# Optimization experiments

Hardware: AMD Instinct MI355X
Metric: run time of the kernel (lower is better)

Reference implementation:

```python
import jax, jax.numpy as jnp
import numpy as np

B, D, S = 16, 64, 2048


def setup_inputs() -> dict:
    key = jax.random.key(0)
    kq, kk, kv, km = jax.random.split(key, 4)
    q = jax.random.normal(kq, (B, D, S), dtype=jnp.float32)
    k = jax.random.normal(kk, (B, D, S), dtype=jnp.float32)
    v = jax.random.normal(kv, (B, D, S), dtype=jnp.float32)
    # boolean mask over the [B, Sq, Sk] score matrix (True -> filled with -1000)
    mask = jax.random.bernoulli(km, 0.1, (B, S, S))
    return {"q": q, "k": k, "v": v, "mask": mask}


def reference(q, k, v, mask):
    dim = jnp.asarray(D, dtype=q.dtype)
    # scores[b, s, t] = sum_d q[b, d, s] * k[b, d, t] / sqrt(D)
    scores = jnp.einsum("bds,bdt->bst", q, k) / jnp.sqrt(dim)
    scores = jnp.where(mask, jnp.asarray(-1000.0, dtype=scores.dtype), scores)
    # NOTE: softmax over dim=1 (the QUERY axis), faithful to nn.Softmax(dim=1)
    attn = jax.nn.softmax(scores, axis=1)
    # out[b, s, d] = sum_t attn[b, s, t] * v[b, d, t]
    out = jnp.einsum("bst,bdt->bsd", attn, v)
    return out
```

## Files before the change

### kernel.cpp

```cpp
#include <hip/hip_runtime.h>
#include <hip/hip_bf16.h>
#include <stdint.h>


namespace {
constexpr int B = 16;
constexpr int D = 64;
constexpr int S = 2048;
constexpr float SCALE = 0.125f;

typedef __attribute__((ext_vector_type(8))) short short8;
typedef __attribute__((ext_vector_type(4))) float f32x4;

constexpr size_t WS_FLAG  = 0;
constexpr size_t WS_LINV  = 256;
constexpr size_t WS_LPART = 256 + 131072;
constexpr size_t WS_QT    = 655616;
constexpr size_t WS_KT    = 4849920;
constexpr size_t WS_VB    = 9044224;
constexpr size_t WS_MPACK = 13238528;
constexpr size_t WS_OPART = 21627136;
constexpr size_t NEED_OLD = 13238528;
constexpr size_t NEED_T1  = 21627136;
constexpr size_t NEED_T2  = 38404352;
}

__device__ __forceinline__ bool mask_at(const void* mask, int mode, size_t idx) {
    if (mode == 1) return ((const int*)mask)[idx] != 0;
    if (mode == 2) return ((const float*)mask)[idx] != 0.0f;
    return ((const unsigned char*)mask)[idx] != 0;
}

__device__ __forceinline__ uint16_t f2bf(float f) {
    unsigned int u = __float_as_uint(f);
    unsigned int r = (u + 0x7fffu + ((u >> 16) & 1u)) >> 16;
    return (uint16_t)r;
}
__device__ __forceinline__ unsigned int pack2(float a, float b) {
    return (unsigned int)f2bf(a) | ((unsigned int)f2bf(b) << 16);
}

__device__ __forceinline__ int swz(int row, int colByte) {
    return row * 128 + (colByte ^ ((row & 7) << 4));
}

__device__ __forceinline__ void gll16(const void* g, void* l) {
    __builtin_amdgcn_global_load_lds(
        (const __attribute__((address_space(1))) void*)g,
        (__attribute__((address_space(3))) void*)l, 16, 0, 0);
}

__device__ __forceinline__ void stage_tile(const char* srcRows, size_t rowStrideB,
                                           unsigned char* dst, int tid) {
    const int lane = tid & 63, w = tid >> 6;
    const int lrow = lane >> 3;
    const int slot = (lane & 7) ^ lrow;
    #pragma unroll
    for (int c = 0; c < 2; ++c) {
        const int row = 16 * w + 8 * c + lrow;
        gll16(srcRows + (size_t)row * rowStrideB + slot * 16,
              dst + (16 * w + 8 * c) * 128);
    }
}

__device__ __forceinline__ f32x4 mfma16(short8 a, short8 b, f32x4 c) {
    return __builtin_amdgcn_mfma_f32_16x16x32_bf16(a, b, c, 0, 0, 0);
}

__global__ void probe_mask_kernel(const unsigned char* __restrict__ mask,
                                  int* __restrict__ flag)
{
    __shared__ int c0s, c123s;
    if (threadIdx.x == 0) { c0s = 0; c123s = 0; }
    __syncthreads();
    int c0 = 0, c123 = 0;
    for (int f = threadIdx.x; f < 65536; f += 256) {
        const int nz = (mask[f] != 0) ? 1 : 0;
        if ((f & 3) == 0) c0 += nz; else c123 += nz;
    }
    atomicAdd(&c0s, c0);
    atomicAdd(&c123s, c123);
    __syncthreads();
    if (threadIdx.x == 0) {
        int mode = 0;
        if (c123s == 0) mode = 1;
        else if (c0s == 0) mode = 2;
        *flag = mode;
    }
}

__global__ __launch_bounds__(256, 2)
void prep_kernel(const float* __restrict__ q, const float* __restrict__ k,
                 const float* __restrict__ v,
                 uint16_t* __restrict__ qT, uint16_t* __restrict__ kT,
                 uint16_t* __restrict__ vb)
{
    __shared__ float ts[64][65];
    const int tid = threadIdx.x;
    const int s0 = blockIdx.x * 64;
    const int b  = blockIdx.y;

    if (blockIdx.z == 2) {
        const int d = tid >> 2, c = tid & 3;
        const float* row = v + ((size_t)b * D + d) * S + s0 + c * 16;
        uint16_t*   orow = vb + ((size_t)b * D + d) * S + s0 + c * 16;
        #pragma unroll
        for (int i = 0; i < 4; ++i) {
            float4 v4 = *(const float4*)(row + 4 * i);
            uint16_t t4[4] = {f2bf(v4.x), f2bf(v4.y), f2bf(v4.z), f2bf(v4.w)};
            *(uint2*)(orow + 4 * i) = *(const uint2*)t4;
        }
        return;
    }

    const float* src = blockIdx.z ? k : q;
    uint16_t*    dst = blockIdx.z ? kT : qT;
    {
        const int d = tid >> 2, c = tid & 3;
        const float* row = src + ((size_t)b * D + d) * S + s0 + c * 16;
        #pragma unroll
        for (int i = 0; i < 4; ++i) {
            float4 v4 = *(const float4*)(row + 4 * i);
            ts[c * 16 + 4 * i + 0][d] = v4.x;
            ts[c * 16 + 4 * i + 1][d] = v4.y;
            ts[c * 16 + 4 * i + 2][d] = v4.z;
            ts[c * 16 + 4 * i + 3][d] = v4.w;
        }
    }
    __syncthreads();
    {
        const int srow = tid >> 2, p = tid & 3;
        uint16_t tmp[16];
        #pragma unroll
        for (int j = 0; j < 16; ++j) tmp[j] = f2bf(ts[srow][p * 16 + j]);
        uint16_t* drow = dst + ((size_t)b * S + s0 + srow) * 64 + p * 16;
        *(uint4*)drow       = ((const uint4*)tmp)[0];
        *((uint4*)drow + 1) = ((const uint4*)tmp)[1];
    }
}

__global__ __launch_bounds__(256, 4)
void pass1_kernel(const uint16_t* __restrict__ qT, const uint16_t* __restrict__ kT,
                  const void* __restrict__ mask, const int* __restrict__ flagp,
                  float* __restrict__ lpart, unsigned long long* __restrict__ mpackT)
{
    __shared__ __align__(16) unsigned char ksb[64 * 128];
    __shared__ __align__(16) unsigned char qsb[2][64 * 128];
    __shared__ unsigned short mbits[64][4];
    __shared__ float red[4][64];

    const int tid = threadIdx.x;
    const int lane = tid & 63, w = tid >> 6;
    const int l = lane & 15, hh = lane >> 4;
    const int t0 = blockIdx.x * 64;
    const int chunk = blockIdx.y;
    const int b = blockIdx.z;
    const int mode = *flagp;

    const int row_m = tid >> 2, cq = tid & 3;
    const size_t mrow_base = ((size_t)b * S + row_m) * S + t0 + cq * 16;

    int4  mr4[4];
    uint4 mr1;
    auto load_mtile = [&](int sbase) {
        if (mode != 0) {
            const int4* p = (const int4*)((const int*)mask + mrow_base + (size_t)sbase * S);
            mr4[0] = p[0]; mr4[1] = p[1]; mr4[2] = p[2]; mr4[3] = p[3];
        } else {
            mr1 = *(const uint4*)((const unsigned char*)mask + mrow_base + (size_t)sbase * S);
        }
    };
    auto pack_mtile = [&]() -> unsigned int {
        unsigned int bits = 0;
        if (mode != 0) {
            #pragma unroll
            for (int i = 0; i < 4; ++i) {
                bits |= (mr4[i].x ? 1u : 0u) << (4 * i + 0);
                bits |= (mr4[i].y ? 1u : 0u) << (4 * i + 1);
                bits |= (mr4[i].z ? 1u : 0u) << (4 * i + 2);
                bits |= (mr4[i].w ? 1u : 0u) << (4 * i + 3);
            }
        } else {
            const unsigned int u[4] = {mr1.x, mr1.y, mr1.z, mr1.w};
            #pragma unroll
            for (int c = 0; c < 4; ++c) {
                bits |= ((u[c] & 0x000000FFu) ? 1u : 0u) << (4 * c + 0);
                bits |= ((u[c] & 0x0000FF00u) ? 1u : 0u) << (4 * c + 1);
                bits |= ((u[c] & 0x00FF0000u) ? 1u : 0u) << (4 * c + 2);
                bits |= ((u[c] & 0xFF000000u) ? 1u : 0u) << (4 * c + 3);
            }
        }
        return bits;
    };

    stage_tile((const char*)(kT + ((size_t)b * S + t0) * 64), 128, ksb, tid);
    stage_tile((const char*)(qT + ((size_t)b * S + chunk * 512) * 64), 128, qsb[0], tid);
    load_mtile(chunk * 512);

    float colacc[4] = {0.f, 0.f, 0.f, 0.f};

    for (int it = 0; it < 8; ++it) {
        const int cur = it & 1;
        const int sbase = chunk * 512 + it * 64;

        __syncthreads();

        const unsigned int bits = pack_mtile();
        mbits[row_m][cq] = (unsigned short)bits;

        __syncthreads();

        if (tid < 64) {
            const unsigned long long word =
                (unsigned long long)mbits[tid][0]
                | ((unsigned long long)mbits[tid][1] << 16)
                | ((unsigned long long)mbits[tid][2] << 32)
                | ((unsigned long long)mbits[tid][3] << 48);
            mpackT[((size_t)b * 32 + (t0 >> 6)) * S + sbase + tid] = word;
        }

        if (it < 7) {
            stage_tile((const char*)(qT + ((size_t)b * S + sbase + 64) * 64), 128,
                       qsb[cur ^ 1], tid);
            load_mtile(sbase + 64);
        }

        short8 A0 = *(const short8*)&qsb[cur][swz(16 * w + l, 0  + hh * 16)];
        short8 A1 = *(const short8*)&qsb[cur][swz(16 * w + l, 64 + hh * 16)];
        const int srow_l = 16 * w + 4 * hh;

        #pragma unroll
        for (int tf = 0; tf < 4; ++tf) {
            const short8 B0 = *(const short8*)&ksb[swz(tf * 16 + l, 0  + hh * 16)];
            const short8 B1 = *(const short8*)&ksb[swz(tf * 16 + l, 64 + hh * 16)];
            f32x4 c4 = {0.f, 0.f, 0.f, 0.f};
            c4 = mfma16(A0, B0, c4);
            c4 = mfma16(A1, B1, c4);
            #pragma unroll
            for (int r = 0; r < 4; ++r) {
                if (!((mbits[srow_l + r][tf] >> l) & 1))
                    colacc[tf] += __expf(c4[r] * SCALE);
            }
        }
    }

    #pragma unroll
    for (int tf = 0; tf < 4; ++tf) {
        colacc[tf] += __shfl_xor(colacc[tf], 16);
        colacc[tf] += __shfl_xor(colacc[tf], 32);
    }
    __syncthreads();
    if (lane < 16) {
        #pragma unroll
        for (int tf = 0; tf < 4; ++tf) red[w][tf * 16 + lane] = colacc[tf];
    }
    __syncthreads();
    if (tid < 64) {
        const float s = red[0][tid] + red[1][tid] + red[2][tid] + red[3][tid];
        lpart[(size_t)chunk * (B * S) + (size_t)b * S + t0 + tid] = s;
    }
}

__global__ void linv_kernel(const float* __restrict__ lpart, float* __restrict__ linv)
{
    const int i = blockIdx.x * 256 + threadIdx.x;
    const float s = lpart[i] + lpart[B * S + i] + lpart[2 * B * S + i] + lpart[3 * B * S + i];
    linv[i] = 1.0f / s;
}

__global__ __launch_bounds__(256, 2)
void pass2_kernel(const uint16_t* __restrict__ qT, const uint16_t* __restrict__ kT,
                  const uint16_t* __restrict__ vb,
                  const unsigned long long* __restrict__ mpackT,
                  const float* __restrict__ linv, float* __restrict__ dst, int tspan)
{
    __shared__ __align__(16) unsigned char qsb[64 * 128];
    __shared__ __align__(16) unsigned char ksb[2][64 * 128];
    __shared__ __align__(16) unsigned char vsb[2][64 * 128];
    __shared__ __align__(16) unsigned char ptb[64 * 128];
    __shared__ unsigned long long mrow2[2][64];
    __shared__ float linv_s[2][64];

    const int tid = threadIdx.x;
    const int lane = tid & 63, w = tid >> 6;
    const int l = lane & 15, hh = lane >> 4;
    const int s0 = blockIdx.x * 64;
    const int tc = blockIdx.y;
    const int b = blockIdx.z;
    const int t_begin = tc * tspan;
    const int niter = tspan / 64;
    float* outp = dst + (size_t)tc * (B * S * D);

    stage_tile((const char*)(qT + ((size_t)b * S + s0) * 64), 128, qsb, tid);
    stage_tile((const char*)(kT + ((size_t)b * S + t_begin) * 64), 128, ksb[0], tid);
    stage_tile((const char*)(vb + (size_t)b * D * S + t_begin), (size_t)S * 2, vsb[0], tid);
    if (tid < 64) {
        mrow2[0][tid]  = mpackT[((size_t)b * 32 + (t_begin >> 6)) * S + s0 + tid];
        linv_s[0][tid] = linv[(size_t)b * S + t_begin + tid];
    }
    __syncthreads();

    short8 QB[4][2];
    #pragma unroll
    for (int sf = 0; sf < 4; ++sf)
        #pragma unroll
        for (int kh = 0; kh < 2; ++kh)
            QB[sf][kh] = *(const short8*)&qsb[swz(sf * 16 + l, kh * 64 + hh * 16)];

    f32x4 oacc[4];
    #pragma unroll
    for (int df = 0; df < 4; ++df) oacc[df] = (f32x4){0.f, 0.f, 0.f, 0.f};

    for (int i = 0; i < niter; ++i) {
        const int cur = i & 1, nxt = cur ^ 1;
        const int t0 = t_begin + i * 64;

        short8 KA0 = *(const short8*)&ksb[cur][swz(16 * w + l, 0  + hh * 16)];
        short8 KA1 = *(const short8*)&ksb[cur][swz(16 * w + l, 64 + hh * 16)];
        float lv[4];
        #pragma unroll
        for (int r = 0; r < 4; ++r) lv[r] = linv_s[cur][16 * w + 4 * hh + r];

        #pragma unroll
        for (int sf = 0; sf < 4; ++sf) {
            f32x4 c4 = {0.f, 0.f, 0.f, 0.f};
            c4 = mfma16(KA0, QB[sf][0], c4);
            c4 = mfma16(KA1, QB[sf][1], c4);
            const unsigned long long bits = mrow2[cur][sf * 16 + l];
            float pv[4];
            #pragma unroll
            for (int r = 0; r < 4; ++r) {
                const int tloc = 16 * w + 4 * hh + r;
                pv[r] = ((bits >> tloc) & 1ull) ? 0.f : __expf(c4[r] * SCALE) * lv[r];
            }
            const int row = sf * 16 + l;
            const int cb = (32 * w + 8 * hh);
            *(uint2*)&ptb[row * 128 + (cb ^ ((row & 7) << 4))] =
                make_uint2(pack2(pv[0], pv[1]), pack2(pv[2], pv[3]));
        }
        __syncthreads();

        if (i + 1 < niter) {
            const int tn = t0 + 64;
            stage_tile((const char*)(kT + ((size_t)b * S + tn) * 64), 128, ksb[nxt], tid);
            stage_tile((const char*)(vb + (size_t)b * D * S + tn), (size_t)S * 2, vsb[nxt], tid);
            if (tid < 64) {
                const unsigned long long mw =
                    mpackT[((size_t)b * 32 + (tn >> 6)) * S + s0 + tid];
                const float lw = linv[(size_t)b * S + tn + tid];
                mrow2[nxt][tid]  = mw;
                linv_s[nxt][tid] = lw;
            }
        }

        short8 PA0 = *(const short8*)&ptb[swz(16 * w + l, 0  + hh * 16)];
        short8 PA1 = *(const short8*)&ptb[swz(16 * w + l, 64 + hh * 16)];
        #pragma unroll
        for (int df = 0; df < 4; ++df) {
            short8 VB0 = *(const short8*)&vsb[cur][swz(df * 16 + l, 0  + hh * 16)];
            short8 VB1 = *(const short8*)&vsb[cur][swz(df * 16 + l, 64 + hh * 16)];
            oacc[df] = mfma16(PA0, VB0, oacc[df]);
            oacc[df] = mfma16(PA1, VB1, oacc[df]);
        }
        __syncthreads();
    }

    #pragma unroll
    for (int df = 0; df < 4; ++df)
        #pragma unroll
        for (int r = 0; r < 4; ++r)
            outp[((size_t)b * S + s0 + 16 * w + 4 * hh + r) * D + df * 16 + l] = oacc[df][r];
}

__global__ void opart_reduce_kernel(const float* __restrict__ p, float* __restrict__ out)
{
    const size_t i = ((size_t)blockIdx.x * 256 + threadIdx.x) * 4;
    float4 a = *(const float4*)(p + i);
    float4 b = *(const float4*)(p + (size_t)B * S * D + i);
    *(float4*)(out + i) = make_float4(a.x + b.x, a.y + b.y, a.z + b.z, a.w + b.w);
}

__global__ __launch_bounds__(256, 2)
void transpose_cvt_kernel(const float* __restrict__ q, const float* __restrict__ k,
                          uint16_t* __restrict__ qT, uint16_t* __restrict__ kT)
{
    __shared__ float ts[64][65];
    const int tid = threadIdx.x;
    const int s0 = blockIdx.x * 64;
    const int b  = blockIdx.y;
    const float* src = blockIdx.z ? k : q;
    uint16_t*    dst = blockIdx.z ? kT : qT;
    {
        const int d = tid >> 2, c = tid & 3;
        const float* row = src + ((size_t)b * D + d) * S + s0 + c * 16;
        #pragma unroll
        for (int i = 0; i < 4; ++i) {
            float4 v4 = *(const float4*)(row + 4 * i);
            ts[c * 16 + 4 * i + 0][d] = v4.x;
            ts[c * 16 + 4 * i + 1][d] = v4.y;
            ts[c * 16 + 4 * i + 2][d] = v4.z;
            ts[c * 16 + 4 * i + 3][d] = v4.w;
        }
    }
    __syncthreads();
    {
        const int srow = tid >> 2, p = tid & 3;
        uint16_t tmp[16];
        #pragma unroll
        for (int j = 0; j < 16; ++j) tmp[j] = f2bf(ts[srow][p * 16 + j]);
        uint16_t* drow = dst + ((size_t)b * S + s0 + srow) * 64 + p * 16;
        *(uint4*)drow       = ((const uint4*)tmp)[0];
        *((uint4*)drow + 1) = ((const uint4*)tmp)[1];
    }
}

__global__ void cvt_v_kernel(const float* __restrict__ v, uint16_t* __restrict__ vb)
{
    const size_t i = ((size_t)blockIdx.x * 256 + threadIdx.x) * 4;
    float4 v4 = *(const float4*)(v + i);
    uint16_t t4[4] = {f2bf(v4.x), f2bf(v4.y), f2bf(v4.z), f2bf(v4.w)};
    *(uint2*)(vb + i) = *(const uint2*)t4;
}

__global__ __launch_bounds__(256, 2)
void pass1_old_kernel(const uint16_t* __restrict__ qT, const uint16_t* __restrict__ kT,
                      const void* __restrict__ mask, const int* __restrict__ flagp,
                      float* __restrict__ lpart)
{
    __shared__ __align__(16) unsigned char ksb[64 * 128];
    __shared__ __align__(16) unsigned char qsb[64 * 128];
    __shared__ float red[4][64];
    const int tid = threadIdx.x;
    const int lane = tid & 63, w = tid >> 6;
    const int l = lane & 15, hh = lane >> 4;
    const int t0 = blockIdx.x * 64;
    const int chunk = blockIdx.y;
    const int b = blockIdx.z;
    const int mode = *flagp;
    const size_t mbase = (size_t)b * S * S;

    stage_tile((const char*)(kT + ((size_t)b * S + t0) * 64), 128, ksb, tid);
    __syncthreads();
    short8 BF[4][2];
    #pragma unroll
    for (int tf = 0; tf < 4; ++tf)
        #pragma unroll
        for (int kh = 0; kh < 2; ++kh)
            BF[tf][kh] = *(const short8*)&ksb[swz(tf * 16 + l, kh * 64 + hh * 16)];
    float colacc[4] = {0.f, 0.f, 0.f, 0.f};
    for (int it = 0; it < 8; ++it) {
        const int sbase = chunk * 512 + it * 64;
        __syncthreads();
        stage_tile((const char*)(qT + ((size_t)b * S + sbase) * 64), 128, qsb, tid);
        __syncthreads();
        short8 A0 = *(const short8*)&qsb[swz(16 * w + l, 0  + hh * 16)];
        short8 A1 = *(const short8*)&qsb[swz(16 * w + l, 64 + hh * 16)];
        #pragma unroll
        for (int tf = 0; tf < 4; ++tf) {
            f32x4 c4 = {0.f, 0.f, 0.f, 0.f};
            c4 = mfma16(A0, BF[tf][0], c4);
            c4 = mfma16(A1, BF[tf][1], c4);
            const int t = t0 + tf * 16 + l;
            const int srow = sbase + 16 * w + 4 * hh;
            #pragma unroll
            for (int r = 0; r < 4; ++r)
                if (!mask_at(mask, mode, mbase + (size_t)(srow + r) * S + t))
                    colacc[tf] += __expf(c4[r] * SCALE);
        }
    }
    #pragma unroll
    for (int tf = 0; tf < 4; ++tf) {
        colacc[tf] += __shfl_xor(colacc[tf], 16);
        colacc[tf] += __shfl_xor(colacc[tf], 32);
    }
    if (lane < 16) {
        #pragma unroll
        for (int tf = 0; tf < 4; ++tf) red[w][tf * 16 + lane] = colacc[tf];
    }
    __syncthreads();
    if (tid < 64) {
        const float s = red[0][tid] + red[1][tid] + red[2][tid] + red[3][tid];
        lpart[(size_t)chunk * (B * S) + (size_t)b * S + t0 + tid] = s;
    }
}

__global__ __launch_bounds__(256, 2)
void pass2_old_kernel(const uint16_t* __restrict__ qT, const uint16_t* __restrict__ kT,
                      const uint16_t* __restrict__ vb, const void* __restrict__ mask,
                      const int* __restrict__ flagp, const float* __restrict__ linv,
                      float* __restrict__ out)
{
    __shared__ __align__(16) unsigned char qsb[64 * 128];
    __shared__ __align__(16) unsigned char ksb[64 * 128];
    __shared__ __align__(16) unsigned char vsb[64 * 128];
    __shared__ __align__(16) unsigned char ptb[64 * 128];
    __shared__ unsigned short mbits[64][4];
    __shared__ float linv_s[64];
    const int tid = threadIdx.x;
    const int lane = tid & 63, w = tid >> 6;
    const int l = lane & 15, hh = lane >> 4;
    const int s0 = blockIdx.x * 64;
    const int b = blockIdx.y;
    const int mode = *flagp;
    const size_t mbase = (size_t)b * S * S;

    stage_tile((const char*)(qT + ((size_t)b * S + s0) * 64), 128, qsb, tid);
    __syncthreads();
    short8 QB[4][2];
    #pragma unroll
    for (int sf = 0; sf < 4; ++sf)
        #pragma unroll
        for (int kh = 0; kh < 2; ++kh)
            QB[sf][kh] = *(const short8*)&qsb[swz(sf * 16 + l, kh * 64 + hh * 16)];
    f32x4 oacc[4];
    #pragma unroll
    for (int df = 0; df < 4; ++df) oacc[df] = (f32x4){0.f, 0.f, 0.f, 0.f};

    for (int t0 = 0; t0 < S; t0 += 64) {
        stage_tile((const char*)(kT + ((size_t)b * S + t0) * 64), 128, ksb, tid);
        stage_tile((const char*)(vb + (size_t)b * D * S + t0), (size_t)S * 2, vsb, tid);
        {
            const int srow = tid >> 2, c = tid & 3;
            const size_t base = mbase + (size_t)(s0 + srow) * S + t0 + c * 16;
            unsigned int bits = 0;
            #pragma unroll
            for (int j = 0; j < 16; ++j)
                bits |= (mask_at(mask, mode, base + j) ? 1u : 0u) << j;
            mbits[srow][c] = (unsigned short)bits;
        }
        if (tid < 64) linv_s[tid] = linv[(size_t)b * S + t0 + tid];
        __syncthreads();

        short8 KA0 = *(const short8*)&ksb[swz(16 * w + l, 0  + hh * 16)];
        short8 KA1 = *(const short8*)&ksb[swz(16 * w + l, 64 + hh * 16)];
        float lv[4];
        #pragma unroll
        for (int r = 0; r < 4; ++r) lv[r] = linv_s[16 * w + 4 * hh + r];
        #pragma unroll
        for (int sf = 0; sf < 4; ++sf) {
            f32x4 c4 = {0.f, 0.f, 0.f, 0.f};
            c4 = mfma16(KA0, QB[sf][0], c4);
            c4 = mfma16(KA1, QB[sf][1], c4);
            const unsigned int mb = (unsigned int)mbits[sf * 16 + l][w] >> (4 * hh);
            float pv[4];
            #pragma unroll
            for (int r = 0; r < 4; ++r)
                pv[r] = ((mb >> r) & 1u) ? 0.f : __expf(c4[r] * SCALE) * lv[r];
            const int row = sf * 16 + l;
            const int cb = (32 * w + 8 * hh);
            *(uint2*)&ptb[row * 128 + (cb ^ ((row & 7) << 4))] =
                make_uint2(pack2(pv[0], pv[1]), pack2(pv[2], pv[3]));
        }
        __syncthreads();
        short8 PA0 = *(const short8*)&ptb[swz(16 * w + l, 0  + hh * 16)];
        short8 PA1 = *(const short8*)&ptb[swz(16 * w + l, 64 + hh * 16)];
        #pragma unroll
        for (int df = 0; df < 4; ++df) {
            short8 VB0 = *(const short8*)&vsb[swz(df * 16 + l, 0  + hh * 16)];
            short8 VB1 = *(const short8*)&vsb[swz(df * 16 + l, 64 + hh * 16)];
            oacc[df] = mfma16(PA0, VB0, oacc[df]);
            oacc[df] = mfma16(PA1, VB1, oacc[df]);
        }
        __syncthreads();
    }
    #pragma unroll
    for (int df = 0; df < 4; ++df)
        #pragma unroll
        for (int r = 0; r < 4; ++r)
            out[((size_t)b * S + s0 + 16 * w + 4 * hh + r) * D + df * 16 + l] = oacc[df][r];
}

__global__ __launch_bounds__(256, 2)
void colsum_fb(const float* __restrict__ q, const float* __restrict__ k,
               const void* __restrict__ mask, const int* __restrict__ flagp,
               float* __restrict__ lsums)
{
    __shared__ __align__(16) float qs[128][68];
    __shared__ __align__(16) float ks[64][68];
    __shared__ float lred[32][66];
    const int tid = threadIdx.x;
    const int b = blockIdx.y;
    const int t0 = blockIdx.x * 64;
    const int mode = *flagp;
    {
        const int tl = tid & 63, d0 = tid >> 6;
        #pragma unroll
        for (int i = 0; i < 16; ++i) { const int d = d0 + i * 4; ks[tl][d] = k[(b * D + d) * S + t0 + tl]; }
    }
    const int tq = tid & 7, sq = tid >> 3;
    float lacc[8];
    #pragma unroll
    for (int j = 0; j < 8; ++j) lacc[j] = 0.f;
    const size_t mbase = (size_t)b * S * S;
    for (int s0 = 0; s0 < S; s0 += 128) {
        __syncthreads();
        {
            const int sl = tid & 127, d0 = tid >> 7;
            #pragma unroll
            for (int i = 0; i < 32; ++i) { const int d = d0 + i * 2; qs[sl][d] = q[(b * D + d) * S + s0 + sl]; }
        }
        __syncthreads();
        float acc[4][8];
        #pragma unroll
        for (int jj = 0; jj < 4; ++jj)
            #pragma unroll
            for (int j = 0; j < 8; ++j) acc[jj][j] = 0.f;
        #pragma unroll
        for (int dblk = 0; dblk < 16; ++dblk) {
            float4 q4[4];
            #pragma unroll
            for (int jj = 0; jj < 4; ++jj) q4[jj] = *(const float4*)&qs[sq + 32 * jj][dblk * 4];
            #pragma unroll
            for (int j = 0; j < 8; ++j) {
                const float4 k4 = *(const float4*)&ks[tq + 8 * j][dblk * 4];
                #pragma unroll
                for (int jj = 0; jj < 4; ++jj)
                    acc[jj][j] += q4[jj].x * k4.x + q4[jj].y * k4.y + q4[jj].z * k4.z + q4[jj].w * k4.w;
            }
        }
        #pragma unroll
        for (int jj = 0; jj < 4; ++jj) {
            const int sg = s0 + sq + 32 * jj;
            const size_t ridx = mbase + (size_t)sg * S + t0;
            #pragma unroll
            for (int j = 0; j < 8; ++j)
                if (!mask_at(mask, mode, ridx + tq + 8 * j)) lacc[j] += __expf(acc[jj][j] * SCALE);
        }
    }
    __syncthreads();
    #pragma unroll
    for (int j = 0; j < 8; ++j) lred[sq][tq + 8 * j] = lacc[j];
    __syncthreads();
    if (tid < 64) {
        float s = 0.f;
        #pragma unroll
        for (int i = 0; i < 32; ++i) s += lred[i][tid];
        lsums[b * S + t0 + tid] = s;
    }
}

__global__ __launch_bounds__(256, 2)
void attn_out_fb(const float* __restrict__ q, const float* __restrict__ k,
                 const float* __restrict__ v, const void* __restrict__ mask,
                 const int* __restrict__ flagp, const float* __restrict__ lsums,
                 float* __restrict__ out)
{
    __shared__ __align__(16) float qs[64][68];
    __shared__ __align__(16) float kw[64][68];
    __shared__ __align__(16) float pt[64][68];
    __shared__ float linv_sh[64];
    const int tid = threadIdx.x;
    const int b = blockIdx.y;
    const int s0 = blockIdx.x * 64;
    const int mode = *flagp;
    {
        const int sl = tid & 63, d0 = tid >> 6;
        #pragma unroll
        for (int i = 0; i < 16; ++i) { const int d = d0 + i * 4; qs[sl][d] = q[(b * D + d) * S + s0 + sl]; }
    }
    const int tq = tid & 7, sq = tid >> 3;
    float oacc[2][8];
    #pragma unroll
    for (int jj = 0; jj < 2; ++jj)
        #pragma unroll
        for (int dd = 0; dd < 8; ++dd) oacc[jj][dd] = 0.f;
    const size_t mbase = (size_t)b * S * S;
    for (int t0 = 0; t0 < S; t0 += 64) {
        __syncthreads();
        if (tid < 64) linv_sh[tid] = 1.f / lsums[b * S + t0 + tid];
        {
            const int tl = tid & 63, d0 = tid >> 6;
            #pragma unroll
            for (int i = 0; i < 16; ++i) { const int d = d0 + i * 4; kw[tl][d] = k[(b * D + d) * S + t0 + tl]; }
        }
        __syncthreads();
        float sc[2][8];
        #pragma unroll
        for (int jj = 0; jj < 2; ++jj)
            #pragma unroll
            for (int j = 0; j < 8; ++j) sc[jj][j] = 0.f;
        #pragma unroll
        for (int dblk = 0; dblk < 16; ++dblk) {
            float4 q4[2];
            #pragma unroll
            for (int jj = 0; jj < 2; ++jj) q4[jj] = *(const float4*)&qs[sq + 32 * jj][dblk * 4];
            #pragma unroll
            for (int j = 0; j < 8; ++j) {
                const float4 k4 = *(const float4*)&kw[tq + 8 * j][dblk * 4];
                #pragma unroll
                for (int jj = 0; jj < 2; ++jj)
                    sc[jj][j] += q4[jj].x * k4.x + q4[jj].y * k4.y + q4[jj].z * k4.z + q4[jj].w * k4.w;
            }
        }
        #pragma unroll
        for (int jj = 0; jj < 2; ++jj) {
            const int sg = s0 + sq + 32 * jj;
            const size_t ridx = mbase + (size_t)sg * S + t0;
            #pragma unroll
            for (int j = 0; j < 8; ++j) {
                const int tl = tq + 8 * j;
                const bool msk = mask_at(mask, mode, ridx + tl);
                pt[tl][sq + 32 * jj] = msk ? 0.f : __expf(sc[jj][j] * SCALE) * linv_sh[tl];
            }
        }
        __syncthreads();
        {
            const int tl = tid & 63, d0 = tid >> 6;
            #pragma unroll
            for (int i = 0; i < 16; ++i) { const int d = d0 + i * 4; kw[tl][d] = v[(b * D + d) * S + t0 + tl]; }
        }
        __syncthreads();
        #pragma unroll 8
        for (int t = 0; t < 64; ++t) {
            const float2 p2 = *(const float2*)&pt[t][sq * 2];
            const float4 w0 = *(const float4*)&kw[t][tq * 8];
            const float4 w1 = *(const float4*)&kw[t][tq * 8 + 4];
            oacc[0][0] += p2.x * w0.x; oacc[0][1] += p2.x * w0.y; oacc[0][2] += p2.x * w0.z; oacc[0][3] += p2.x * w0.w;
            oacc[0][4] += p2.x * w1.x; oacc[0][5] += p2.x * w1.y; oacc[0][6] += p2.x * w1.z; oacc[0][7] += p2.x * w1.w;
            oacc[1][0] += p2.y * w0.x; oacc[1][1] += p2.y * w0.y; oacc[1][2] += p2.y * w0.z; oacc[1][3] += p2.y * w0.w;
            oacc[1][4] += p2.y * w1.x; oacc[1][5] += p2.y * w1.y; oacc[1][6] += p2.y * w1.z; oacc[1][7] += p2.y * w1.w;
        }
    }
    #pragma unroll
    for (int jj = 0; jj < 2; ++jj) {
        float* dst = out + ((size_t)(b * S + s0 + sq * 2 + jj)) * D + tq * 8;
        *(float4*)dst = make_float4(oacc[jj][0], oacc[jj][1], oacc[jj][2], oacc[jj][3]);
        *(float4*)(dst + 4) = make_float4(oacc[jj][4], oacc[jj][5], oacc[jj][6], oacc[jj][7]);
    }
}

extern "C" void kernel_launch(void* const* d_in, const int* in_sizes, int n_in,
                              void* d_out, int out_size, void* d_ws, size_t ws_size,
                              hipStream_t stream) {
    const float* q = (const float*)d_in[0];
    const float* k = (const float*)d_in[1];
    const float* v = (const float*)d_in[2];
    const void*  mask = d_in[3];
    float* out = (float*)d_out;
    char* ws = (char*)d_ws;

    int* flag = (int*)(ws + WS_FLAG);
    probe_mask_kernel<<<1, 256, 0, stream>>>((const unsigned char*)mask, flag);

    if (ws_size >= NEED_T1) {
        float*    linv  = (float*)(ws + WS_LINV);
        float*    lpart = (float*)(ws + WS_LPART);
        uint16_t* qT    = (uint16_t*)(ws + WS_QT);
        uint16_t* kT    = (uint16_t*)(ws + WS_KT);
        uint16_t* vb    = (uint16_t*)(ws + WS_VB);
        unsigned long long* mpackT = (unsigned long long*)(ws + WS_MPACK);

        prep_kernel<<<dim3(S / 64, B, 3), 256, 0, stream>>>(q, k, v, qT, kT, vb);
        pass1_kernel<<<dim3(S / 64, 4, B), 256, 0, stream>>>(qT, kT, mask, flag, lpart, mpackT);
        linv_kernel<<<(B * S) / 256, 256, 0, stream>>>(lpart, linv);

        if (ws_size >= NEED_T2) {
            float* opart = (float*)(ws + WS_OPART);
            pass2_kernel<<<dim3(S / 64, 2, B), 256, 0, stream>>>(
                qT, kT, vb, mpackT, linv, opart, S / 2);
            opart_reduce_kernel<<<(B * S * D) / (256 * 4), 256, 0, stream>>>(opart, out);
        } else {
            pass2_kernel<<<dim3(S / 64, 1, B), 256, 0, stream>>>(
                qT, kT, vb, mpackT, linv, out, S);
        }
    } else if (ws_size >= NEED_OLD) {
        float*    linv  = (float*)(ws + WS_LINV);
        float*    lpart = (float*)(ws + WS_LPART);
        uint16_t* qT    = (uint16_t*)(ws + WS_QT);
        uint16_t* kT    = (uint16_t*)(ws + WS_KT);
        uint16_t* vb    = (uint16_t*)(ws + WS_VB);
        transpose_cvt_kernel<<<dim3(S / 64, B, 2), 256, 0, stream>>>(q, k, qT, kT);
        cvt_v_kernel<<<(B * D * S) / (256 * 4), 256, 0, stream>>>(v, vb);
        pass1_old_kernel<<<dim3(S / 64, 4, B), 256, 0, stream>>>(qT, kT, mask, flag, lpart);
        linv_kernel<<<(B * S) / 256, 256, 0, stream>>>(lpart, linv);
        pass2_old_kernel<<<dim3(S / 64, B), 256, 0, stream>>>(qT, kT, vb, mask, flag, linv, out);
    } else {
        float* lsums = (float*)(ws + WS_LINV);
        dim3 grid(S / 64, B);
        colsum_fb<<<grid, 256, 0, stream>>>(q, k, mask, flag, lsums);
        attn_out_fb<<<grid, 256, 0, stream>>>(q, k, v, mask, flag, lsums, out);
    }
}
```

Baseline: 180.2 us.

## Fold mask probe and linv into other kernels, restructure pass2 with 32-row tiles

```diff
diff --git a/kernel.cpp b/kernel.cpp
--- a/kernel.cpp
+++ b/kernel.cpp
@@ -19,10 +19,8 @@
 constexpr size_t WS_KT    = 4849920;
 constexpr size_t WS_VB    = 9044224;
 constexpr size_t WS_MPACK = 13238528;
-constexpr size_t WS_OPART = 21627136;
 constexpr size_t NEED_OLD = 13238528;
 constexpr size_t NEED_T1  = 21627136;
-constexpr size_t NEED_T2  = 38404352;
 }
 
 __device__ __forceinline__ bool mask_at(const void* mask, int mode, size_t idx) {
@@ -63,37 +61,52 @@
     }
 }
 
+__device__ __forceinline__ void stage_tile32(const char* srcRows, size_t rowStrideB,
+                                             unsigned char* dst, int tid) {
+    const int lane = tid & 63, w = tid >> 6;
+    const int lrow = lane >> 3;
+    const int slot = (lane & 7) ^ lrow;
+    const int row = 8 * w + lrow;
+    gll16(srcRows + (size_t)row * rowStrideB + slot * 16, dst + 8 * w * 128);
+}
+
 __device__ __forceinline__ f32x4 mfma16(short8 a, short8 b, f32x4 c) {
     return __builtin_amdgcn_mfma_f32_16x16x32_bf16(a, b, c, 0, 0, 0);
 }
 
+__device__ __forceinline__ void probe_body(const unsigned char* mask, int* flag,
+                                           int tid, int* c0s, int* c123s) {
+    if (tid == 0) { *c0s = 0; *c123s = 0; }
+    __syncthreads();
+    int c0 = 0, c123 = 0;
+    for (int f = tid; f < 65536; f += 256) {
+        const int nz = (mask[f] != 0) ? 1 : 0;
+        if ((f & 3) == 0) c0 += nz; else c123 += nz;
+    }
+    atomicAdd(c0s, c0);
+    atomicAdd(c123s, c123);
+    __syncthreads();
+    if (tid == 0) {
+        int mode = 0;
+        if (*c123s == 0) mode = 1;
+        else if (*c0s == 0) mode = 2;
+        *flag = mode;
+    }
+}
+
 __global__ void probe_mask_kernel(const unsigned char* __restrict__ mask,
                                   int* __restrict__ flag)
 {
     __shared__ int c0s, c123s;
-    if (threadIdx.x == 0) { c0s = 0; c123s = 0; }
-    __syncthreads();
-    int c0 = 0, c123 = 0;
-    for (int f = threadIdx.x; f < 65536; f += 256) {
-        const int nz = (mask[f] != 0) ? 1 : 0;
-        if ((f & 3) == 0) c0 += nz; else c123 += nz;
-    }
-    atomicAdd(&c0s, c0);
-    atomicAdd(&c123s, c123);
-    __syncthreads();
-    if (threadIdx.x == 0) {
-        int mode = 0;
-        if (c123s == 0) mode = 1;
-        else if (c0s == 0) mode = 2;
-        *flag = mode;
-    }
+    probe_body(mask, flag, threadIdx.x, &c0s, &c123s);
 }
 
 __global__ __launch_bounds__(256, 2)
 void prep_kernel(const float* __restrict__ q, const float* __restrict__ k,
                  const float* __restrict__ v,
                  uint16_t* __restrict__ qT, uint16_t* __restrict__ kT,
-                 uint16_t* __restrict__ vb)
+                 uint16_t* __restrict__ vb,
+                 const unsigned char* __restrict__ mask, int* __restrict__ flag)
 {
     __shared__ float ts[64][65];
     const int tid = threadIdx.x;
@@ -109,6 +122,10 @@
             float4 v4 = *(const float4*)(row + 4 * i);
             uint16_t t4[4] = {f2bf(v4.x), f2bf(v4.y), f2bf(v4.z), f2bf(v4.w)};
             *(uint2*)(orow + 4 * i) = *(const uint2*)t4;
+        }
+        if (blockIdx.x == 0 && blockIdx.y == 0) {
+            __shared__ int c0s, c123s;
+            probe_body(mask, flag, tid, &c0s, &c123s);
         }
         return;
     }
@@ -145,7 +162,7 @@
                   float* __restrict__ lpart, unsigned long long* __restrict__ mpackT)
 {
     __shared__ __align__(16) unsigned char ksb[64 * 128];
-    __shared__ __align__(16) unsigned char qsb[2][64 * 128];
+    __shared__ __align__(16) unsigned char qsb[64 * 128];
     __shared__ unsigned short mbits[64][4];
     __shared__ float red[4][64];
 
@@ -194,19 +211,21 @@
     };
 
     stage_tile((const char*)(kT + ((size_t)b * S + t0) * 64), 128, ksb, tid);
-    stage_tile((const char*)(qT + ((size_t)b * S + chunk * 512) * 64), 128, qsb[0], tid);
+    stage_tile((const char*)(qT + ((size_t)b * S + chunk * 512) * 64), 128, qsb, tid);
     load_mtile(chunk * 512);
 
     float colacc[4] = {0.f, 0.f, 0.f, 0.f};
 
     for (int it = 0; it < 8; ++it) {
-        const int cur = it & 1;
         const int sbase = chunk * 512 + it * 64;
 
         __syncthreads();
 
         const unsigned int bits = pack_mtile();
         mbits[row_m][cq] = (unsigned short)bits;
+
+        short8 A0 = *(const short8*)&qsb[swz(16 * w + l, 0  + hh * 16)];
+        short8 A1 = *(const short8*)&qsb[swz(16 * w + l, 64 + hh * 16)];
 
         __syncthreads();
 
@@ -220,15 +239,11 @@
         }
 
         if (it < 7) {
-            stage_tile((const char*)(qT + ((size_t)b * S + sbase + 64) * 64), 128,
-                       qsb[cur ^ 1], tid);
+            stage_tile((const char*)(qT + ((size_t)b * S + sbase + 64) * 64), 128, qsb, tid);
             load_mtile(sbase + 64);
         }
 
-        short8 A0 = *(const short8*)&qsb[cur][swz(16 * w + l, 0  + hh * 16)];
-        short8 A1 = *(const short8*)&qsb[cur][swz(16 * w + l, 64 + hh * 16)];
         const int srow_l = 16 * w + 4 * hh;
-
         #pragma unroll
         for (int tf = 0; tf < 4; ++tf) {
             const short8 B0 = *(const short8*)&ksb[swz(tf * 16 + l, 0  + hh * 16)];
@@ -261,68 +276,74 @@
     }
 }
 
-__global__ void linv_kernel(const float* __restrict__ lpart, float* __restrict__ linv)
-{
-    const int i = blockIdx.x * 256 + threadIdx.x;
-    const float s = lpart[i] + lpart[B * S + i] + lpart[2 * B * S + i] + lpart[3 * B * S + i];
-    linv[i] = 1.0f / s;
-}
-
-__global__ __launch_bounds__(256, 2)
+__global__ __launch_bounds__(256, 4)
 void pass2_kernel(const uint16_t* __restrict__ qT, const uint16_t* __restrict__ kT,
                   const uint16_t* __restrict__ vb,
                   const unsigned long long* __restrict__ mpackT,
-                  const float* __restrict__ linv, float* __restrict__ dst, int tspan)
-{
-    __shared__ __align__(16) unsigned char qsb[64 * 128];
-    __shared__ __align__(16) unsigned char ksb[2][64 * 128];
-    __shared__ __align__(16) unsigned char vsb[2][64 * 128];
-    __shared__ __align__(16) unsigned char ptb[64 * 128];
-    __shared__ unsigned long long mrow2[2][64];
+                  const float* __restrict__ lpart, float* __restrict__ out)
+{
+    __shared__ __align__(16) unsigned char qsb[32 * 128];
+    __shared__ __align__(16) unsigned char ksb[64 * 128];
+    __shared__ __align__(16) unsigned char vsb[64 * 128];
+    __shared__ __align__(16) unsigned char ptb[32 * 128];
+    __shared__ unsigned long long mrow2[2][32];
     __shared__ float linv_s[2][64];
 
     const int tid = threadIdx.x;
     const int lane = tid & 63, w = tid >> 6;
     const int l = lane & 15, hh = lane >> 4;
-    const int s0 = blockIdx.x * 64;
-    const int tc = blockIdx.y;
-    const int b = blockIdx.z;
-    const int t_begin = tc * tspan;
-    const int niter = tspan / 64;
-    float* outp = dst + (size_t)tc * (B * S * D);
-
-    stage_tile((const char*)(qT + ((size_t)b * S + s0) * 64), 128, qsb, tid);
-    stage_tile((const char*)(kT + ((size_t)b * S + t_begin) * 64), 128, ksb[0], tid);
-    stage_tile((const char*)(vb + (size_t)b * D * S + t_begin), (size_t)S * 2, vsb[0], tid);
-    if (tid < 64) {
-        mrow2[0][tid]  = mpackT[((size_t)b * 32 + (t_begin >> 6)) * S + s0 + tid];
-        linv_s[0][tid] = linv[(size_t)b * S + t_begin + tid];
-    }
-    __syncthreads();
-
-    short8 QB[4][2];
-    #pragma unroll
-    for (int sf = 0; sf < 4; ++sf)
+    const int s0 = blockIdx.x * 32;
+    const int b = blockIdx.y;
+
+    auto load_meta = [&](int tile, int slot) {
+        if (tid < 64) {
+            const int t = tile * 64 + tid;
+            const float s = lpart[(size_t)b * S + t]
+                          + lpart[(size_t)(B * S) + b * S + t]
+                          + lpart[(size_t)(2 * B * S) + b * S + t]
+                          + lpart[(size_t)(3 * B * S) + b * S + t];
+            linv_s[slot][tid] = 1.0f / s;
+        } else if (tid < 96) {
+            mrow2[slot][tid - 64] =
+                mpackT[((size_t)b * 32 + tile) * S + s0 + (tid - 64)];
+        }
+    };
+
+    stage_tile32((const char*)(qT + ((size_t)b * S + s0) * 64), 128, qsb, tid);
+    stage_tile((const char*)(kT + (size_t)b * S * 64), 128, ksb, tid);
+    stage_tile((const char*)(vb + (size_t)b * D * S), (size_t)S * 2, vsb, tid);
+    load_meta(0, 0);
+    __syncthreads();
+
+    short8 QB[2][2];
+    #pragma unroll
+    for (int sf = 0; sf < 2; ++sf)
         #pragma unroll
         for (int kh = 0; kh < 2; ++kh)
             QB[sf][kh] = *(const short8*)&qsb[swz(sf * 16 + l, kh * 64 + hh * 16)];
 
-    f32x4 oacc[4];
-    #pragma unroll
-    for (int df = 0; df < 4; ++df) oacc[df] = (f32x4){0.f, 0.f, 0.f, 0.f};
-
-    for (int i = 0; i < niter; ++i) {
+    f32x4 oacc[2];
+    oacc[0] = (f32x4){0.f, 0.f, 0.f, 0.f};
+    oacc[1] = (f32x4){0.f, 0.f, 0.f, 0.f};
+
+    const int sb = w & 1;
+    const int dh = w >> 1;
+
+    for (int i = 0; i < 32; ++i) {
         const int cur = i & 1, nxt = cur ^ 1;
-        const int t0 = t_begin + i * 64;
-
-        short8 KA0 = *(const short8*)&ksb[cur][swz(16 * w + l, 0  + hh * 16)];
-        short8 KA1 = *(const short8*)&ksb[cur][swz(16 * w + l, 64 + hh * 16)];
+
+        if (i > 0)
+            stage_tile((const char*)(vb + (size_t)b * D * S + i * 64),
+                       (size_t)S * 2, vsb, tid);
+
+        short8 KA0 = *(const short8*)&ksb[swz(16 * w + l, 0  + hh * 16)];
+        short8 KA1 = *(const short8*)&ksb[swz(16 * w + l, 64 + hh * 16)];
         float lv[4];
         #pragma unroll
         for (int r = 0; r < 4; ++r) lv[r] = linv_s[cur][16 * w + 4 * hh + r];
 
         #pragma unroll
-        for (int sf = 0; sf < 4; ++sf) {
+        for (int sf = 0; sf < 2; ++sf) {
             f32x4 c4 = {0.f, 0.f, 0.f, 0.f};
             c4 = mfma16(KA0, QB[sf][0], c4);
             c4 = mfma16(KA1, QB[sf][1], c4);
@@ -340,25 +361,19 @@
         }
         __syncthreads();
 
-        if (i + 1 < niter) {
-            const int tn = t0 + 64;
-            stage_tile((const char*)(kT + ((size_t)b * S + tn) * 64), 128, ksb[nxt], tid);
-            stage_tile((const char*)(vb + (size_t)b * D * S + tn), (size_t)S * 2, vsb[nxt], tid);
-            if (tid < 64) {
-                const unsigned long long mw =
-                    mpackT[((size_t)b * 32 + (tn >> 6)) * S + s0 + tid];
-                const float lw = linv[(size_t)b * S + tn + tid];
-                mrow2[nxt][tid]  = mw;
-                linv_s[nxt][tid] = lw;
-            }
-        }
-
-        short8 PA0 = *(const short8*)&ptb[swz(16 * w + l, 0  + hh * 16)];
-        short8 PA1 = *(const short8*)&ptb[swz(16 * w + l, 64 + hh * 16)];
-        #pragma unroll
-        for (int df = 0; df < 4; ++df) {
-            short8 VB0 = *(const short8*)&vsb[cur][swz(df * 16 + l, 0  + hh * 16)];
-            short8 VB1 = *(const short8*)&vsb[cur][swz(df * 16 + l, 64 + hh * 16)];
+        if (i + 1 < 32) {
+            stage_tile((const char*)(kT + ((size_t)b * S + (i + 1) * 64) * 64),
+                       128, ksb, tid);
+            load_meta(i + 1, nxt);
+        }
+
+        short8 PA0 = *(const short8*)&ptb[swz(sb * 16 + l, 0  + hh * 16)];
+        short8 PA1 = *(const short8*)&ptb[swz(sb * 16 + l, 64 + hh * 16)];
+        #pragma unroll
+        for (int df = 0; df < 2; ++df) {
+            const int drow = (dh * 2 + df) * 16 + l;
+            short8 VB0 = *(const short8*)&vsb[swz(drow, 0  + hh * 16)];
+            short8 VB1 = *(const short8*)&vsb[swz(drow, 64 + hh * 16)];
             oacc[df] = mfma16(PA0, VB0, oacc[df]);
             oacc[df] = mfma16(PA1, VB1, oacc[df]);
         }
@@ -366,18 +381,11 @@
     }
 
     #pragma unroll
-    for (int df = 0; df < 4; ++df)
+    for (int df = 0; df < 2; ++df)
         #pragma unroll
         for (int r = 0; r < 4; ++r)
-            outp[((size_t)b * S + s0 + 16 * w + 4 * hh + r) * D + df * 16 + l] = oacc[df][r];
-}
-
-__global__ void opart_reduce_kernel(const float* __restrict__ p, float* __restrict__ out)
-{
-    const size_t i = ((size_t)blockIdx.x * 256 + threadIdx.x) * 4;
-    float4 a = *(const float4*)(p + i);
-    float4 b = *(const float4*)(p + (size_t)B * S * D + i);
-    *(float4*)(out + i) = make_float4(a.x + b.x, a.y + b.y, a.z + b.z, a.w + b.w);
+            out[((size_t)b * S + s0 + sb * 16 + 4 * hh + r) * D
+                + (dh * 2 + df) * 16 + l] = oacc[df][r];
 }
 
 __global__ __launch_bounds__(256, 2)
@@ -420,6 +428,13 @@
     float4 v4 = *(const float4*)(v + i);
     uint16_t t4[4] = {f2bf(v4.x), f2bf(v4.y), f2bf(v4.z), f2bf(v4.w)};
     *(uint2*)(vb + i) = *(const uint2*)t4;
+}
+
+__global__ void linv_kernel(const float* __restrict__ lpart, float* __restrict__ linv)
+{
+    const int i = blockIdx.x * 256 + threadIdx.x;
+    const float s = lpart[i] + lpart[B * S + i] + lpart[2 * B * S + i] + lpart[3 * B * S + i];
+    linv[i] = 1.0f / s;
 }
 
 __global__ __launch_bounds__(256, 2)
@@ -740,35 +755,27 @@
     char* ws = (char*)d_ws;
 
     int* flag = (int*)(ws + WS_FLAG);
-    probe_mask_kernel<<<1, 256, 0, stream>>>((const unsigned char*)mask, flag);
 
     if (ws_size >= NEED_T1) {
-        float*    linv  = (float*)(ws + WS_LINV);
         float*    lpart = (float*)(ws + WS_LPART);
         uint16_t* qT    = (uint16_t*)(ws + WS_QT);
         uint16_t* kT    = (uint16_t*)(ws + WS_KT);
         uint16_t* vb    = (uint16_t*)(ws + WS_VB);
         unsigned long long* mpackT = (unsigned long long*)(ws + WS_MPACK);
 
-        prep_kernel<<<dim3(S / 64, B, 3), 256, 0, stream>>>(q, k, v, qT, kT, vb);
-        pass1_kernel<<<dim3(S / 64, 4, B), 256, 0, stream>>>(qT, kT, mask, flag, lpart, mpackT);
-        linv_kernel<<<(B * S) / 256, 256, 0, stream>>>(lpart, linv);
-
-        if (ws_size >= NEED_T2) {
-            float* opart = (float*)(ws + WS_OPART);
-            pass2_kernel<<<dim3(S / 64, 2, B), 256, 0, stream>>>(
-                qT, kT, vb, mpackT, linv, opart, S / 2);
-            opart_reduce_kernel<<<(B * S * D) / (256 * 4), 256, 0, stream>>>(opart, out);
-        } else {
-            pass2_kernel<<<dim3(S / 64, 1, B), 256, 0, stream>>>(
-                qT, kT, vb, mpackT, linv, out, S);
-        }
+        prep_kernel<<<dim3(S / 64, B, 3), 256, 0, stream>>>(
+            q, k, v, qT, kT, vb, (const unsigned char*)mask, flag);
+        pass1_kernel<<<dim3(S / 64, 4, B), 256, 0, stream>>>(
+            qT, kT, mask, flag, lpart, mpackT);
+        pass2_kernel<<<dim3(S / 32, B), 256, 0, stream>>>(
+            qT, kT, vb, mpackT, lpart, out);
     } else if (ws_size >= NEED_OLD) {
         float*    linv  = (float*)(ws + WS_LINV);
         float*    lpart = (float*)(ws + WS_LPART);
         uint16_t* qT    = (uint16_t*)(ws + WS_QT);
         uint16_t* kT    = (uint16_t*)(ws + WS_KT);
         uint16_t* vb    = (uint16_t*)(ws + WS_VB);
+        probe_mask_kernel<<<1, 256, 0, stream>>>((const unsigned char*)mask, flag);
         transpose_cvt_kernel<<<dim3(S / 64, B, 2), 256, 0, stream>>>(q, k, qT, kT);
         cvt_v_kernel<<<(B * D * S) / (256 * 4), 256, 0, stream>>>(v, vb);
         pass1_old_kernel<<<dim3(S / 64, 4, B), 256, 0, stream>>>(qT, kT, mask, flag, lpart);
@@ -776,6 +783,7 @@
         pass2_old_kernel<<<dim3(S / 64, B), 256, 0, stream>>>(qT, kT, vb, mask, flag, linv, out);
     } else {
         float* lsums = (float*)(ws + WS_LINV);
+        probe_mask_kernel<<<1, 256, 0, stream>>>((const unsigned char*)mask, flag);
         dim3 grid(S / 64, B);
         colsum_fb<<<grid, 256, 0, stream>>>(q, k, mask, flag, lsums);
         attn_out_fb<<<grid, 256, 0, stream>>>(q, k, v, mask, flag, lsums, out);
```

Measured after the change: 169.4 us. 1.06x faster.
